# Kernel optimization log

Hardware: AMD Instinct MI355X
Metric: run time of the kernel (lower is better)

Reference implementation:

```python
import jax, jax.numpy as jnp
import numpy as np

B = 8192        # number of drug-cell pairs (graphs)
NPG = 32        # nodes per graph
EPG = 64        # directed edges per graph
N = B * NPG     # total nodes
E = B * EPG     # total edges
CELL = 908      # cell_inp_dim
BN_EPS = 1e-5


def _bn(x):
    # BatchNorm1d in training mode with gamma=1, beta=0 (fresh init), biased var
    m = x.mean(0)
    v = x.var(0)
    return (x - m) * jax.lax.rsqrt(v + BN_EPS)


def _lin_params(k, fan_in, fan_out):
    kw, _ = jax.random.split(k)
    w = jax.random.normal(kw, (fan_in, fan_out), jnp.float32) / np.sqrt(fan_in)
    b = jnp.zeros((fan_out,), jnp.float32)
    return w, b


_DIMS = [("ce_1", CELL, 516), ("ce_2", 516, 256), ("ce_3", 256, 128),
         ("g1_1", 9, 128), ("g1_2", 128, 128),
         ("g2_1", 128, 128), ("g2_2", 128, 128),
         ("d_1", 128, 128), ("d_2", 128, 128),
         ("f_1", 256, 128), ("f_2", 128, 64), ("f_3", 64, 1)]


def setup_inputs() -> dict:
    key = jax.random.key(0)
    ks = jax.random.split(key, 4 + len(_DIMS))
    inp = {}
    inp["cell"] = jax.random.normal(ks[0], (B, CELL), jnp.float32)
    inp["drug_x"] = jax.random.normal(ks[1], (N, 9), jnp.float32)
    g = jnp.arange(E) // EPG  # graph id per edge
    src = g * NPG + jax.random.randint(ks[2], (E,), 0, NPG)
    dst = g * NPG + jax.random.randint(ks[3], (E,), 0, NPG)
    inp["drug_edge_index"] = jnp.stack([src, dst]).astype(jnp.int32)
    inp["drug_batch"] = (jnp.arange(N) // NPG).astype(jnp.int32)
    for i, (nm, a, b) in enumerate(_DIMS):
        w, bb = _lin_params(ks[4 + i], a, b)
        inp[nm + "_w"] = w
        inp[nm + "_b"] = bb
    return inp


def _forward(cell, drug_x, src, dst, batch,
             ce_1_w, ce_1_b, ce_2_w, ce_2_b, ce_3_w, ce_3_b,
             g1_1_w, g1_1_b, g1_2_w, g1_2_b,
             g2_1_w, g2_1_b, g2_2_w, g2_2_b,
             d_1_w, d_1_b, d_2_w, d_2_b,
             f_1_w, f_1_b, f_2_w, f_2_b, f_3_w, f_3_b):
    # cell_emb branch (dropout = identity in eval/reference)
    c = jax.nn.relu(_bn(cell @ ce_1_w + ce_1_b))
    c = jax.nn.relu(_bn(c @ ce_2_w + ce_2_b))
    c = jax.nn.relu(_bn(c @ ce_3_w + ce_3_b))

    # GINConv 1: h = MLP((1+eps)*x + sum_{j in N(i)} x_j), eps=0
    agg = jax.ops.segment_sum(drug_x[src], dst, num_segments=N)
    h = drug_x + agg
    h = jax.nn.relu(_bn(h @ g1_1_w + g1_1_b)) @ g1_2_w + g1_2_b  # inner MLP: Lin-BN-ReLU-Lin
    h = _bn(jax.nn.relu(h))  # outer ReLU then BN (per Sequential order)

    # GINConv 2
    agg = jax.ops.segment_sum(h[src], dst, num_segments=N)
    h = h + agg
    h = jax.nn.relu(_bn(h @ g2_1_w + g2_1_b)) @ g2_2_w + g2_2_b
    h = _bn(jax.nn.relu(h))

    # global max pool over nodes of each graph -> [B, 128]
    p = jax.ops.segment_max(h, batch, num_segments=B)

    d = jax.nn.relu(_bn(p @ d_1_w + d_1_b))
    d = jax.nn.relu(d @ d_2_w + d_2_b)

    z = jnp.concatenate([c, d], axis=-1)  # [B, 256]
    z = jax.nn.elu(_bn(z @ f_1_w + f_1_b))
    z = jax.nn.elu(_bn(z @ f_2_w + f_2_b))
    y = (z @ f_3_w + f_3_b).reshape(B)
    return y


def reference(cell, drug_x, drug_edge_index, drug_batch,
              ce_1_w, ce_1_b, ce_2_w, ce_2_b, ce_3_w, ce_3_b,
              g1_1_w, g1_1_b, g1_2_w, g1_2_b,
              g2_1_w, g2_1_b, g2_2_w, g2_2_b,
              d_1_w, d_1_b, d_2_w, d_2_b,
              f_1_w, f_1_b, f_2_w, f_2_b, f_3_w, f_3_b):
    src, dst = drug_edge_index[0], drug_edge_index[1]
    return _forward(cell, drug_x, src, dst, drug_batch,
                    ce_1_w, ce_1_b, ce_2_w, ce_2_b, ce_3_w, ce_3_b,
                    g1_1_w, g1_1_b, g1_2_w, g1_2_b,
                    g2_1_w, g2_1_b, g2_2_w, g2_2_b,
                    d_1_w, d_1_b, d_2_w, d_2_b,
                    f_1_w, f_1_b, f_2_w, f_2_b, f_3_w, f_3_b)
```

## Files before the change

### kernel.cpp

```cpp
#include <hip/hip_runtime.h>
#include <hip/hip_bf16.h>
#include <math.h>

#define BGRAPH 8192
#define NPG 32
#define EPG 64
#define NNODE (BGRAPH * NPG)
#define NEDGE (BGRAPH * EPG)
#define CELLD 908
#define BN_EPS 1e-5f
#define ABF_STR 960
#define C1_STR 576

typedef __attribute__((ext_vector_type(8))) short bf16x8;
typedef __attribute__((ext_vector_type(4))) float f32x4;
typedef __attribute__((ext_vector_type(4))) unsigned short us4;
typedef __attribute__((ext_vector_type(8))) unsigned short us8;

__device__ __forceinline__ unsigned short f2bf(float f)
{
    unsigned int u = __float_as_uint(f);
    u = (u + 0x7FFFu + ((u >> 16) & 1u)) >> 16;
    return (unsigned short)u;
}

__device__ __forceinline__ bf16x8 quant8(const float v[8])
{
    union { bf16x8 b; unsigned short u[8]; } fr;
    #pragma unroll
    for (int j = 0; j < 8; ++j) fr.u[j] = f2bf(v[j]);
    return fr.b;
}

__device__ __forceinline__ void bf2f8(bf16x8 b, float v[8])
{
    union { bf16x8 bb; unsigned short u[8]; } x; x.bb = b;
    #pragma unroll
    for (int j = 0; j < 8; ++j) v[j] = __uint_as_float((unsigned)x.u[j] << 16);
}

__device__ __forceinline__ float apply_in(float v, int mode, float mn, float iv)
{
    if (mode == 1)      { v = (v - mn) * iv; v = fmaxf(v, 0.f); }
    else if (mode == 2) { v = (v - mn) * iv; v = (v > 0.f) ? v : expm1f(v); }
    else if (mode == 3) { v = fmaxf(v, 0.f); v = (v - mn) * iv; }
    return v;
}

struct TransArgs {
    const float* w[11];
    unsigned short* wt[11];
    int K[11], N[11], ntN[11];
    int off[12];
};

__global__ void transpose_w(TransArgs a)
{
    __shared__ float t[64][65];
    int b = blockIdx.x, tid = threadIdx.x;
    int s = 0;
    while (s < 10 && b >= a.off[s + 1]) ++s;
    int t0 = b - a.off[s];
    int K = a.K[s], N = a.N[s], ntn = a.ntN[s];
    int kt = t0 / ntn, nt = t0 - kt * ntn;
    int k0 = kt * 64, n0 = nt * 64;
    const float* w = a.w[s];
    unsigned short* wt = a.wt[s];
    int c = tid & 63, rg = tid >> 6;
    #pragma unroll
    for (int i = 0; i < 16; ++i) {
        int rr = rg * 16 + i;
        int k = k0 + rr, n = n0 + c;
        t[c][rr] = (k < K && n < N) ? w[(size_t)k * N + n] : 0.f;
    }
    __syncthreads();
    #pragma unroll
    for (int i = 0; i < 16; ++i) {
        int rr = rg * 16 + i;
        int n = n0 + rr, k = k0 + c;
        if (n < N && k < K) wt[(size_t)n * K + k] = f2bf(t[rr][c]);
    }
}

struct SetupArgs {
    float* zb; int zTotal; int zBlocks;
    const int* src; const int* dst; int* row_start; int* col_idx;
};

__global__ void setup_all(SetupArgs a)
{
    int b = blockIdx.x;
    int tid = threadIdx.x;
    if (b < a.zBlocks) {
        int i = b * 256 + tid;
        if (i < a.zTotal) a.zb[i] = 0.f;
        return;
    }
    b -= a.zBlocks;
    __shared__ int cnt[4][32], fill[4][32], rsl[4][33];
    int gl = tid >> 6, e = tid & 63;
    int g = b * 4 + gl;
    if (e < 32) { cnt[gl][e] = 0; fill[gl][e] = 0; }
    __syncthreads();
    int s = a.src[g * EPG + e] - g * NPG;
    int d = a.dst[g * EPG + e] - g * NPG;
    atomicAdd(&cnt[gl][d], 1);
    __syncthreads();
    if (e == 0) {
        int acc = 0;
        for (int i = 0; i < 32; ++i) { rsl[gl][i] = acc; acc += cnt[gl][i]; }
        rsl[gl][32] = acc;
    }
    __syncthreads();
    int pos = rsl[gl][d] + atomicAdd(&fill[gl][d], 1);
    a.col_idx[g * EPG + pos] = s;
    if (e < 33) a.row_start[g * 33 + e] = rsl[gl][e];
}

__global__ void quant_cell(const float* __restrict__ cell, unsigned short* __restrict__ abf)
{
    int i = blockIdx.x * 256 + threadIdx.x;
    int row = i / (ABF_STR / 4), c4 = i - row * (ABF_STR / 4);
    int k = c4 * 4;
    us4 w = (us4){0, 0, 0, 0};
    if (k < CELLD) {
        float4 f = *(const float4*)&cell[(size_t)row * CELLD + k];
        w = (us4){ f2bf(f.x), f2bf(f.y), f2bf(f.z), f2bf(f.w) };
    }
    *(us4*)&abf[(size_t)row * ABF_STR + k] = w;
}

__global__ void quant_c1(const float* __restrict__ c1, const float* __restrict__ stats,
                         float inv_sM, unsigned short* __restrict__ out)
{
    int i = blockIdx.x * 256 + threadIdx.x;
    int row = i / (C1_STR / 4), c4 = i - row * (C1_STR / 4);
    int k = c4 * 4;
    us4 w = (us4){0, 0, 0, 0};
    if (k < 516) {
        float4 f = *(const float4*)&c1[(size_t)row * 516 + k];
        float v[4] = {f.x, f.y, f.z, f.w};
        #pragma unroll
        for (int j = 0; j < 4; ++j) {
            float s = stats[k + j], ss = stats[516 + k + j];
            float mn = s * inv_sM;
            float iv = rsqrtf(ss * inv_sM - mn * mn + BN_EPS);
            v[j] = fmaxf((v[j] - mn) * iv, 0.f);
        }
        w = (us4){ f2bf(v[0]), f2bf(v[1]), f2bf(v[2]), f2bf(v[3]) };
    }
    *(us4*)&out[(size_t)row * C1_STR + k] = w;
}

__global__ void reduce_stats(const float* __restrict__ part, int nrows, int nt,
                             float* __restrict__ out)
{
    int c = threadIdx.x;
    int per = nrows >> 6;
    int r0 = blockIdx.x * per;
    bool isq = (c >= 128);
    int cc = isq ? c - 128 : c;
    if (cc >= nt) return;
    float s = 0.f;
    for (int r = 0; r < per; ++r) s += part[(size_t)(r0 + r) * 256 + c];
    unsafeAtomicAdd(&out[(isq ? nt : 0) + cc], s);
}

#define HBS 136

__launch_bounds__(256)
__global__ void gin_s1(const float* __restrict__ drug_x,
                       const int* __restrict__ row_start,
                       const int* __restrict__ col_idx,
                       const unsigned short* __restrict__ W11,
                       const float* __restrict__ b11,
                       unsigned short* uout,
                       float* __restrict__ part)
{
    __shared__ __align__(16) unsigned short h[4 * 32 * HBS];
    __shared__ __align__(16) unsigned char ubuf[4096];
    __shared__ int rs[4][36];
    __shared__ int ci[4][64];

    unsigned short* w11l = (unsigned short*)ubuf;
    float* red = (float*)ubuf;

    int tid  = threadIdx.x;
    int wave = tid >> 6;
    int lane = tid & 63;
    int quad = lane >> 4;
    int l16  = lane & 15;
    int g0   = blockIdx.x * 4;
    unsigned short* hw = h + wave * (32 * HBS);
    float* xw = (float*)hw;

    for (int i = tid; i < 128 * 16; i += 256) {
        int n = i >> 4, k = i & 15;
        w11l[i] = (k < 9) ? W11[n * 9 + k] : (unsigned short)0;
    }
    if (tid < 132) {
        int gl = tid / 33, idx = tid - gl * 33;
        rs[gl][idx] = row_start[(g0 + gl) * 33 + idx];
    }
    {
        int gl = tid >> 6, e = tid & 63;
        ci[gl][e] = col_idx[(g0 + gl) * EPG + e];
    }
    {
        const float* xg = drug_x + (size_t)(g0 + wave) * 32 * 9;
        for (int i = lane; i < 32 * 16; i += 64) {
            int rr = i >> 4, c = i & 15;
            xw[i] = (c < 9) ? xg[rr * 9 + c] : 0.f;
        }
    }
    __syncthreads();

    f32x4 acc[2][8];
    #pragma unroll
    for (int i = 0; i < 2; ++i)
        #pragma unroll
        for (int j = 0; j < 8; ++j)
            acc[i][j] = (f32x4){0.f, 0.f, 0.f, 0.f};

    {
        bf16x8 af[2];
        #pragma unroll
        for (int mt = 0; mt < 2; ++mt) {
            int rowl = mt * 16 + l16;
            float v[8] = {0, 0, 0, 0, 0, 0, 0, 0};
            if (quad < 2) {
                float4 lo = *(const float4*)&xw[rowl * 16 + quad * 8];
                float4 hi = *(const float4*)&xw[rowl * 16 + quad * 8 + 4];
                v[0] = lo.x; v[1] = lo.y; v[2] = lo.z; v[3] = lo.w;
                v[4] = hi.x; v[5] = hi.y; v[6] = hi.z; v[7] = hi.w;
                int e0 = rs[wave][rowl], e1 = rs[wave][rowl + 1];
                for (int e = e0; e < e1; ++e) {
                    int sr = ci[wave][e];
                    float4 l2 = *(const float4*)&xw[sr * 16 + quad * 8];
                    float4 h2 = *(const float4*)&xw[sr * 16 + quad * 8 + 4];
                    v[0] += l2.x; v[1] += l2.y; v[2] += l2.z; v[3] += l2.w;
                    v[4] += h2.x; v[5] += h2.y; v[6] += h2.z; v[7] += h2.w;
                }
            }
            af[mt] = quant8(v);
        }
        #pragma unroll
        for (int nt = 0; nt < 8; ++nt) {
            bf16x8 b;
            if (quad < 2) b = *(const bf16x8*)(const void*)&w11l[(nt * 16 + l16) * 16 + quad * 8];
            else { float z[8] = {0,0,0,0,0,0,0,0}; b = quant8(z); }
            acc[0][nt] = __builtin_amdgcn_mfma_f32_16x16x32_bf16(af[0], b, acc[0][nt], 0, 0, 0);
            acc[1][nt] = __builtin_amdgcn_mfma_f32_16x16x32_bf16(af[1], b, acc[1][nt], 0, 0, 0);
        }
    }

    float ls[8], lq[8];
    unsigned short* ub = uout + (size_t)(g0 + wave) * 32 * 128;
    #pragma unroll
    for (int nt = 0; nt < 8; ++nt) {
        int col = nt * 16 + l16;
        float bv = b11[col];
        float s0 = 0.f, q0 = 0.f;
        #pragma unroll
        for (int mt = 0; mt < 2; ++mt) {
            int rb = mt * 16 + quad * 4;
            #pragma unroll
            for (int r = 0; r < 4; ++r) {
                float u = acc[mt][nt][r] + bv;
                ub[(size_t)(rb + r) * 128 + col] = f2bf(u);
                s0 += u; q0 += u * u;
            }
        }
        ls[nt] = s0; lq[nt] = q0;
    }
    __syncthreads();
    #pragma unroll
    for (int nt = 0; nt < 8; ++nt) {
        float s = ls[nt], q = lq[nt];
        s += __shfl_xor(s, 16); q += __shfl_xor(q, 16);
        s += __shfl_xor(s, 32); q += __shfl_xor(q, 32);
        if (quad == 0) {
            int col = nt * 16 + l16;
            red[(wave * 2 + 0) * 128 + col] = s;
            red[(wave * 2 + 1) * 128 + col] = q;
        }
    }
    __syncthreads();
    if (tid < 128) {
        float s = red[0 * 128 + tid] + red[2 * 128 + tid] + red[4 * 128 + tid] + red[6 * 128 + tid];
        float q = red[1 * 128 + tid] + red[3 * 128 + tid] + red[5 * 128 + tid] + red[7 * 128 + tid];
        part[(size_t)blockIdx.x * 256 + tid] = s;
        part[(size_t)blockIdx.x * 256 + 128 + tid] = q;
    }
}

__launch_bounds__(256)
__global__ void gin_s3f(const unsigned short* __restrict__ uin,
                        const int* __restrict__ row_start,
                        const int* __restrict__ col_idx,
                        const unsigned short* __restrict__ Wt,
                        const float* __restrict__ bias,
                        const float* __restrict__ in_stats, float inv_sM,
                        unsigned short* __restrict__ uout,
                        float* __restrict__ part)
{
    __shared__ __align__(16) unsigned short wsl[128 * 136];
    __shared__ float pmv[256];
    __shared__ int rs[2][33];
    __shared__ int ci[2][64];
    float* zt = (float*)wsl;

    int tid  = threadIdx.x;
    int wave = tid >> 6;
    int lane = tid & 63;
    int quad = lane >> 4;
    int l16  = lane & 15;
    int g0   = blockIdx.x * 2;
    int row0 = blockIdx.x * 64;

    if (tid < 128) {
        float s = in_stats[tid], ss = in_stats[128 + tid];
        float mn = s * inv_sM;
        pmv[tid] = mn;
        pmv[128 + tid] = rsqrtf(ss * inv_sM - mn * mn + BN_EPS);
    }
    if (tid < 66) {
        int gl = tid / 33, idx = tid - gl * 33;
        rs[gl][idx] = row_start[(g0 + gl) * 33 + idx];
    }
    if (tid >= 128) {
        int t = tid - 128;
        ci[t >> 6][t & 63] = col_idx[(g0 + (t >> 6)) * EPG + (t & 63)];
    }
    for (int i = tid; i < 128 * 32; i += 256) {
        int n = i >> 5, k = (i & 31) * 4;
        *(us4*)&wsl[n * 136 + k] = *(const us4*)&Wt[(size_t)n * 128 + k];
    }
    __syncthreads();

    bf16x8 afrag[4];
    {
        const unsigned short* ap = uin + (size_t)(row0 + wave * 16 + l16) * 128;
        #pragma unroll
        for (int ks = 0; ks < 4; ++ks) {
            int kb = ks * 32 + quad * 8;
            float v[8];
            bf2f8(*(const bf16x8*)(const void*)&ap[kb], v);
            #pragma unroll
            for (int j = 0; j < 8; ++j)
                v[j] = (fmaxf(v[j], 0.f) - pmv[kb + j]) * pmv[128 + kb + j];
            afrag[ks] = quant8(v);
        }
    }

    f32x4 acc[8];
    #pragma unroll
    for (int j = 0; j < 8; ++j) acc[j] = (f32x4){0.f, 0.f, 0.f, 0.f};
    #pragma unroll
    for (int ks = 0; ks < 4; ++ks) {
        int kb = ks * 32 + quad * 8;
        #pragma unroll
        for (int nt = 0; nt < 8; ++nt) {
            bf16x8 b = *(const bf16x8*)(const void*)&wsl[(nt * 16 + l16) * 136 + kb];
            acc[nt] = __builtin_amdgcn_mfma_f32_16x16x32_bf16(afrag[ks], b, acc[nt], 0, 0, 0);
        }
    }
    __syncthreads();

    #pragma unroll
    for (int nt = 0; nt < 8; ++nt) {
        int col = nt * 16 + l16;
        #pragma unroll
        for (int r = 0; r < 4; ++r)
            zt[(wave * 16 + quad * 4 + r) * 132 + col] = acc[nt][r];
    }
    __syncthreads();

    float sv[4] = {0.f, 0.f, 0.f, 0.f}, qv[4] = {0.f, 0.f, 0.f, 0.f};
    {
        int c4  = (tid & 31) * 4;
        int rg  = tid >> 5;
        int hh  = rg >> 2;
        int rb0 = (rg & 3) * 8;
        float4 bv = *(const float4*)&bias[c4];
        unsigned short* ub = uout + (size_t)row0 * 128;
        for (int rr = 0; rr < 8; ++rr) {
            int r = rb0 + rr;
            int lr = hh * 32 + r;
            float4 val = *(const float4*)&zt[lr * 132 + c4];
            int e0 = rs[hh][r], e1 = rs[hh][r + 1];
            for (int e = e0; e < e1; ++e) {
                float4 zz = *(const float4*)&zt[(hh * 32 + ci[hh][e]) * 132 + c4];
                val.x += zz.x; val.y += zz.y; val.z += zz.z; val.w += zz.w;
            }
            float u0 = val.x + bv.x, u1 = val.y + bv.y;
            float u2 = val.z + bv.z, u3 = val.w + bv.w;
            *(us4*)&ub[(size_t)lr * 128 + c4] =
                (us4){ f2bf(u0), f2bf(u1), f2bf(u2), f2bf(u3) };
            sv[0] += u0; sv[1] += u1; sv[2] += u2; sv[3] += u3;
            qv[0] += u0 * u0; qv[1] += u1 * u1; qv[2] += u2 * u2; qv[3] += u3 * u3;
        }
    }
    __syncthreads();
    {
        int c4 = (tid & 31) * 4, rg = tid >> 5;
        #pragma unroll
        for (int j = 0; j < 4; ++j) {
            zt[rg * 128 + c4 + j] = sv[j];
            zt[1024 + rg * 128 + c4 + j] = qv[j];
        }
    }
    __syncthreads();
    if (tid < 128) {
        float s = 0.f, q = 0.f;
        #pragma unroll
        for (int rg = 0; rg < 8; ++rg) {
            s += zt[rg * 128 + tid];
            q += zt[1024 + rg * 128 + tid];
        }
        part[(size_t)blockIdx.x * 256 + tid] = s;
        part[(size_t)blockIdx.x * 256 + 128 + tid] = q;
    }
}

template<int DO_POOL>
__launch_bounds__(256)
__global__ void gin_lin(const unsigned short* __restrict__ uin,
                        const unsigned short* __restrict__ Wt,
                        const float* __restrict__ bias,
                        const float* __restrict__ in_stats, float inv_sM,
                        unsigned short* uout,
                        float* __restrict__ part,
                        float* __restrict__ pool_out)
{
    __shared__ __align__(16) unsigned short Ws_l[128 * 136];
    __shared__ float pmv[256];
    __shared__ float red[4][2][128];

    int tid  = threadIdx.x;
    int wave = tid >> 6;
    int lane = tid & 63;
    int quad = lane >> 4;
    int l16  = lane & 15;
    int row0 = blockIdx.x * 64;

    for (int i = tid; i < 128 * 32; i += 256) {
        int n = i >> 5, k = (i & 31) * 4;
        *(us4*)&Ws_l[n * 136 + k] = *(const us4*)&Wt[(size_t)n * 128 + k];
    }
    if (tid < 128) {
        float s = in_stats[tid], ss = in_stats[128 + tid];
        float mn = s * inv_sM;
        pmv[tid] = mn;
        pmv[128 + tid] = rsqrtf(ss * inv_sM - mn * mn + BN_EPS);
    }
    __syncthreads();

    bf16x8 afrag[4];
    {
        const unsigned short* ap = uin + (size_t)(row0 + wave * 16 + l16) * 128;
        #pragma unroll
        for (int ks = 0; ks < 4; ++ks) {
            int kb = ks * 32 + quad * 8;
            float v[8];
            bf2f8(*(const bf16x8*)(const void*)&ap[kb], v);
            #pragma unroll
            for (int j = 0; j < 8; ++j)
                v[j] = fmaxf((v[j] - pmv[kb + j]) * pmv[128 + kb + j], 0.f);
            afrag[ks] = quant8(v);
        }
    }

    f32x4 acc[8];
    #pragma unroll
    for (int j = 0; j < 8; ++j) acc[j] = (f32x4){0.f, 0.f, 0.f, 0.f};
    #pragma unroll
    for (int ks = 0; ks < 4; ++ks) {
        int kb = ks * 32 + quad * 8;
        #pragma unroll
        for (int nt = 0; nt < 8; ++nt) {
            bf16x8 b = *(const bf16x8*)(const void*)&Ws_l[(nt * 16 + l16) * 136 + kb];
            acc[nt] = __builtin_amdgcn_mfma_f32_16x16x32_bf16(afrag[ks], b, acc[nt], 0, 0, 0);
        }
    }

    float ls[8], lq[8], lm[8];
    #pragma unroll
    for (int nt = 0; nt < 8; ++nt) {
        int col = nt * 16 + l16;
        float bv = bias[col];
        int rb = row0 + wave * 16 + quad * 4;
        float s0 = 0.f, q0 = 0.f, mx = -INFINITY;
        #pragma unroll
        for (int r = 0; r < 4; ++r) {
            float u = acc[nt][r] + bv;
            float ru = fmaxf(u, 0.f);
            s0 += ru; q0 += ru * ru;
            if (DO_POOL) mx = fmaxf(mx, ru);
            else uout[(size_t)(rb + r) * 128 + col] = f2bf(u);
        }
        ls[nt] = s0; lq[nt] = q0; lm[nt] = mx;
    }

    #pragma unroll
    for (int nt = 0; nt < 8; ++nt) {
        float s = ls[nt], q = lq[nt];
        s += __shfl_xor(s, 16); q += __shfl_xor(q, 16);
        s += __shfl_xor(s, 32); q += __shfl_xor(q, 32);
        if (quad == 0) {
            red[wave][0][nt * 16 + l16] = s;
            red[wave][1][nt * 16 + l16] = q;
        }
    }
    __syncthreads();
    if (tid < 128) {
        float s = red[0][0][tid] + red[1][0][tid] + red[2][0][tid] + red[3][0][tid];
        float q = red[0][1][tid] + red[1][1][tid] + red[2][1][tid] + red[3][1][tid];
        part[(size_t)blockIdx.x * 256 + tid] = s;
        part[(size_t)blockIdx.x * 256 + 128 + tid] = q;
    }
    if (DO_POOL) {
        __syncthreads();
        #pragma unroll
        for (int nt = 0; nt < 8; ++nt) {
            float m = lm[nt];
            m = fmaxf(m, __shfl_xor(m, 16));
            m = fmaxf(m, __shfl_xor(m, 32));
            if (quad == 0) red[wave][0][nt * 16 + l16] = m;
        }
        __syncthreads();
        {
            int gi = tid >> 7, col = tid & 127;
            float m = fmaxf(red[gi * 2][0][col], red[gi * 2 + 1][0][col]);
            pool_out[(size_t)((row0 >> 5) + gi) * 128 + col] = m;
        }
    }
}

template<int KSTEPS, int NT>
__launch_bounds__(256)
__global__ void gemm_rB(const float* __restrict__ A, const float* __restrict__ A2,
                        int lda, int K, int stats_K, int ksplit,
                        const unsigned short* __restrict__ Wt,
                        const float* __restrict__ bias, float* __restrict__ C,
                        const float* __restrict__ in_stats, float inv_sM, int in_mode,
                        float* __restrict__ part, int stats_mode, int out_act)
{
    constexpr int LSTRW = KSTEPS * 32 + 8;
    constexpr int NSUBW = NT / 64;
    __shared__ unsigned short Ws_l[NT * LSTRW];
    __shared__ float pm[KSTEPS * 32], pv[KSTEPS * 32];

    int tid  = threadIdx.x;
    int wave = tid >> 6;
    int lane = tid & 63;
    int quad = lane >> 4;
    int l16  = lane & 15;
    int m0   = blockIdx.x * 16;

    for (int i = tid; i < NT * (KSTEPS * 8); i += 256) {
        int n = i / (KSTEPS * 8), g4 = i % (KSTEPS * 8);
        int k = g4 * 4;
        us4 w = (us4){0, 0, 0, 0};
        if (k < K) w = *(const us4*)(Wt + (size_t)n * K + k);
        *(us4*)&Ws_l[n * LSTRW + k] = w;
    }
    if (in_mode) {
        for (int k = tid; k < KSTEPS * 32; k += 256) {
            float mn = 0.f, iv = 1.f;
            if (k < stats_K) {
                float s = in_stats[k], ss = in_stats[stats_K + k];
                mn = s * inv_sM;
                float vr = ss * inv_sM - mn * mn;
                iv = rsqrtf(vr + BN_EPS);
            }
            pm[k] = mn; pv[k] = iv;
        }
    }
    __syncthreads();

    bf16x8 afrag[KSTEPS];
    {
        int row = m0 + l16;
        const float* ap = A + (size_t)row * lda;
        #pragma unroll
        for (int ks = 0; ks < KSTEPS; ++ks) {
            int kb = ks * 32 + quad * 8;
            float v[8];
            #pragma unroll
            for (int hh = 0; hh < 2; ++hh) {
                int k = kb + hh * 4;
                const float* p = (k >= ksplit) ? &A2[(size_t)row * 128 + (k - 128)]
                                               : &ap[k];
                float4 f = *(const float4*)p;
                v[hh * 4 + 0] = f.x; v[hh * 4 + 1] = f.y;
                v[hh * 4 + 2] = f.z; v[hh * 4 + 3] = f.w;
            }
            if (in_mode) {
                #pragma unroll
                for (int j = 0; j < 8; ++j)
                    v[j] = apply_in(v[j], in_mode, pm[kb + j], pv[kb + j]);
            }
            afrag[ks] = quant8(v);
        }
    }

    f32x4 acc[NSUBW];
    #pragma unroll
    for (int j = 0; j < NSUBW; ++j) acc[j] = (f32x4){0.f, 0.f, 0.f, 0.f};

    #pragma unroll
    for (int ks = 0; ks < KSTEPS; ++ks) {
        #pragma unroll
        for (int nt = 0; nt < NSUBW; ++nt) {
            bf16x8 b = *(const bf16x8*)(const void*)
                &Ws_l[((wave * NSUBW + nt) * 16 + l16) * LSTRW + ks * 32 + quad * 8];
            acc[nt] = __builtin_amdgcn_mfma_f32_16x16x32_bf16(afrag[ks], b, acc[nt], 0, 0, 0);
        }
    }

    float ls[NSUBW], lq[NSUBW];
    #pragma unroll
    for (int nt = 0; nt < NSUBW; ++nt) { ls[nt] = 0.f; lq[nt] = 0.f; }

    #pragma unroll
    for (int nt = 0; nt < NSUBW; ++nt) {
        int col = (wave * NSUBW + nt) * 16 + l16;
        float bv = bias[col];
        int rbase = m0 + quad * 4;
        #pragma unroll
        for (int r = 0; r < 4; ++r) {
            float u = acc[nt][r] + bv;
            if (C) {
                float wv = out_act ? fmaxf(u, 0.f) : u;
                C[(size_t)(rbase + r) * NT + col] = wv;
            }
            if (stats_mode) {
                float s = (stats_mode == 2) ? fmaxf(u, 0.f) : u;
                ls[nt] += s; lq[nt] += s * s;
            }
        }
    }

    if (stats_mode) {
        #pragma unroll
        for (int nt = 0; nt < NSUBW; ++nt) {
            float s = ls[nt], q = lq[nt];
            s += __shfl_xor(s, 16); q += __shfl_xor(q, 16);
            s += __shfl_xor(s, 32); q += __shfl_xor(q, 32);
            if (quad == 0) {
                int col = (wave * NSUBW + nt) * 16 + l16;
                part[(size_t)blockIdx.x * 256 + col] = s;
                part[(size_t)blockIdx.x * 256 + 128 + col] = q;
            }
        }
    }
}

template<int NT, int ABF>
__launch_bounds__(256)
__global__ void gemm_cell(const float* __restrict__ A,
                          const unsigned short* __restrict__ Abf, int abf_str,
                          const unsigned short* __restrict__ Wt,
                          const float* __restrict__ bias, float* __restrict__ C,
                          int M, int K, int N,
                          const float* __restrict__ in_stats, float inv_sM, int in_mode,
                          float* __restrict__ out_stats)
{
    constexpr int NSUB = NT / 16;
    constexpr int PMSZ = ABF ? 1 : 916;
    __shared__ unsigned short As_l[64 * 72];
    __shared__ unsigned short Ws_l[NT * 72];
    __shared__ float pm[PMSZ], pv[PMSZ];
    __shared__ float red[4][2][NT];

    int tid = threadIdx.x;
    int wave = tid >> 6;
    int lane = tid & 63;
    int quad = lane >> 4;
    int l16 = lane & 15;
    int m0 = blockIdx.x * 64, n0 = blockIdx.y * NT;

    if (!ABF && in_mode) {
        for (int k = tid; k < K; k += 256) {
            float s = in_stats[k], ss = in_stats[K + k];
            float mn = s * inv_sM;
            float vr = ss * inv_sM - mn * mn;
            pm[k] = mn; pv[k] = rsqrtf(vr + BN_EPS);
        }
        __syncthreads();
    }

    f32x4 acc[NSUB];
    #pragma unroll
    for (int j = 0; j < NSUB; ++j) acc[j] = (f32x4){0.f, 0.f, 0.f, 0.f};

    for (int k0 = 0; k0 < K; k0 += 64) {
        if (ABF) {
            #pragma unroll
            for (int t = 0; t < 2; ++t) {
                int i = t * 256 + tid;
                int row = i >> 3, c8 = (i & 7) * 8;
                us8 w = *(const us8*)&Abf[(size_t)(m0 + row) * abf_str + k0 + c8];
                *(us8*)&As_l[row * 72 + c8] = w;
            }
        } else {
            for (int i = tid; i < 64 * 16; i += 256) {
                int row = i >> 4, f4 = i & 15;
                int k = k0 + f4 * 4;
                us4 w4 = (us4){0, 0, 0, 0};
                if (k < K) {
                    float4 f = *(const float4*)&A[(size_t)(m0 + row) * K + k];
                    if (in_mode) {
                        f.x = apply_in(f.x, in_mode, pm[k], pv[k]);
                        f.y = apply_in(f.y, in_mode, pm[k + 1], pv[k + 1]);
                        f.z = apply_in(f.z, in_mode, pm[k + 2], pv[k + 2]);
                        f.w = apply_in(f.w, in_mode, pm[k + 3], pv[k + 3]);
                    }
                    w4 = (us4){ f2bf(f.x), f2bf(f.y), f2bf(f.z), f2bf(f.w) };
                }
                *(us4*)&As_l[row * 72 + f4 * 4] = w4;
            }
        }
        for (int i = tid; i < NT * 16; i += 256) {
            int nn = i >> 4, kt = i & 15;
            int k = k0 + kt * 4;
            int gn = n0 + nn;
            us4 w4 = (us4){0, 0, 0, 0};
            if (gn < N && k < K) w4 = *(const us4*)&Wt[(size_t)gn * K + k];
            *(us4*)&Ws_l[nn * 72 + kt * 4] = w4;
        }
        __syncthreads();
        int rowb = wave * 16;
        #pragma unroll
        for (int ks = 0; ks < 2; ++ks) {
            bf16x8 a = *(const bf16x8*)(const void*)&As_l[(rowb + l16) * 72 + ks * 32 + quad * 8];
            #pragma unroll
            for (int nt = 0; nt < NSUB; ++nt) {
                bf16x8 b = *(const bf16x8*)(const void*)&Ws_l[(nt * 16 + l16) * 72 + ks * 32 + quad * 8];
                acc[nt] = __builtin_amdgcn_mfma_f32_16x16x32_bf16(a, b, acc[nt], 0, 0, 0);
            }
        }
        __syncthreads();
    }

    float ls[NSUB], lq[NSUB];
    #pragma unroll
    for (int nt = 0; nt < NSUB; ++nt) { ls[nt] = 0.f; lq[nt] = 0.f; }

    #pragma unroll
    for (int nt = 0; nt < NSUB; ++nt) {
        int col = n0 + nt * 16 + l16;
        if (col < N) {
            float bv = bias[col];
            int rbase = m0 + wave * 16 + quad * 4;
            #pragma unroll
            for (int r = 0; r < 4; ++r) {
                float u = acc[nt][r] + bv;
                C[(size_t)(rbase + r) * N + col] = u;
                ls[nt] += u; lq[nt] += u * u;
            }
        }
    }

    #pragma unroll
    for (int nt = 0; nt < NSUB; ++nt) {
        float s = ls[nt], q = lq[nt];
        s += __shfl_xor(s, 16); q += __shfl_xor(q, 16);
        s += __shfl_xor(s, 32); q += __shfl_xor(q, 32);
        if (quad == 0) { red[wave][0][nt * 16 + l16] = s; red[wave][1][nt * 16 + l16] = q; }
    }
    __syncthreads();
    if (tid < NT) {
        int col = n0 + tid;
        if (col < N) {
            float s = red[0][0][tid] + red[1][0][tid] + red[2][0][tid] + red[3][0][tid];
            float q = red[0][1][tid] + red[1][1][tid] + red[2][1][tid] + red[3][1][tid];
            unsafeAtomicAdd(&out_stats[col], s);
            unsafeAtomicAdd(&out_stats[N + col], q);
        }
    }
}

__global__ void final_dot(const float* __restrict__ u, const float* __restrict__ w,
                          const float* __restrict__ b, float* __restrict__ y,
                          const float* __restrict__ stats, float inv_sM)
{
    __shared__ float pmv[64], piv[64], sw[64];
    int tid = threadIdx.x;
    if (tid < 64) {
        float s = stats[tid], ss = stats[64 + tid];
        float mn = s * inv_sM;
        float vr = ss * inv_sM - mn * mn;
        pmv[tid] = mn;
        piv[tid] = rsqrtf(vr + BN_EPS);
        sw[tid] = w[tid];
    }
    __syncthreads();
    int i = blockIdx.x * blockDim.x + tid;
    if (i >= BGRAPH) return;
    float acc = 0.f;
    #pragma unroll
    for (int k = 0; k < 64; ++k) {
        float v = (u[(size_t)i * 64 + k] - pmv[k]) * piv[k];
        v = (v > 0.f) ? v : expm1f(v);
        acc += v * sw[k];
    }
    y[i] = acc + b[0];
}

extern "C" void kernel_launch(void* const* d_in, const int* in_sizes, int n_in,
                              void* d_out, int out_size, void* d_ws, size_t ws_size,
                              hipStream_t stream)
{
    const float* cell   = (const float*)d_in[0];
    const float* drug_x = (const float*)d_in[1];
    const int*   eidx   = (const int*)d_in[2];
    const float* ce1w = (const float*)d_in[4];  const float* ce1b = (const float*)d_in[5];
    const float* ce2w = (const float*)d_in[6];  const float* ce2b = (const float*)d_in[7];
    const float* ce3w = (const float*)d_in[8];  const float* ce3b = (const float*)d_in[9];
    const float* g11w = (const float*)d_in[10]; const float* g11b = (const float*)d_in[11];
    const float* g12w = (const float*)d_in[12]; const float* g12b = (const float*)d_in[13];
    const float* g21w = (const float*)d_in[14]; const float* g21b = (const float*)d_in[15];
    const float* g22w = (const float*)d_in[16]; const float* g22b = (const float*)d_in[17];
    const float* d1w  = (const float*)d_in[18]; const float* d1b  = (const float*)d_in[19];
    const float* d2w  = (const float*)d_in[20]; const float* d2b  = (const float*)d_in[21];
    const float* f1w  = (const float*)d_in[22]; const float* f1b  = (const float*)d_in[23];
    const float* f2w  = (const float*)d_in[24]; const float* f2b  = (const float*)d_in[25];
    const float* f3w  = (const float*)d_in[26]; const float* f3b  = (const float*)d_in[27];

    const int* src = eidx;
    const int* dst = eidx + NEDGE;
    float* out = (float*)d_out;

    const float INV_N = 1.f / (float)NNODE;
    const float INV_B = 1.f / (float)BGRAPH;
    const int KBIG = 1 << 30;

    float* ws = (float*)d_ws;
    unsigned short* ubg = (unsigned short*)ws;
    float* pbuf = ws + (size_t)NNODE * 64;
    float* sb   = pbuf + (size_t)BGRAPH * 128;
    unsigned short* wtb = (unsigned short*)(sb + 10 * 1032);
    auto ST = [&](int i) { return sb + (size_t)i * 1032; };
    float* st_u1    = ST(0);
    float* st_u2rel = ST(1);
    float* st_u3    = ST(2);
    float* st_u4rel = ST(3);
    float* st_c1    = ST(4);
    float* st_c2    = ST(5);
    float* st_c3    = ST(6);
    float* st_d1    = ST(7);
    float* st_f1    = ST(8);
    float* st_f2    = ST(9);

    float* c1    = ws;
    float* c2    = c1 + (size_t)BGRAPH * 516;
    float* c3u   = c2 + (size_t)BGRAPH * 256;
    float* dbuf  = c3u + (size_t)BGRAPH * 128;
    float* d2buf = dbuf + (size_t)BGRAPH * 128;
    float* f1o   = d2buf + (size_t)BGRAPH * 128;
    float* f2o   = f1o + (size_t)BGRAPH * 128;

    struct WDef { const float* w; int K; int N; };
    WDef wd[11] = {
        {ce1w, CELLD, 516}, {ce2w, 516, 256}, {ce3w, 256, 128},
        {g11w, 9, 128}, {g12w, 128, 128}, {g21w, 128, 128}, {g22w, 128, 128},
        {d1w, 128, 128}, {d2w, 128, 128}, {f1w, 256, 128}, {f2w, 128, 64}
    };
    TransArgs ta;
    int off = 0;
    unsigned short* wt[11];
    ta.off[0] = 0;
    for (int i = 0; i < 11; ++i) {
        wt[i] = wtb + off;
        ta.w[i] = wd[i].w; ta.wt[i] = wt[i];
        ta.K[i] = wd[i].K; ta.N[i] = wd[i].N;
        ta.ntN[i] = (wd[i].N + 63) / 64;
        ta.off[i + 1] = ta.off[i] + ((wd[i].K + 63) / 64) * ta.ntN[i];
        off += wd[i].K * wd[i].N;
    }

    SetupArgs sa;
    sa.zb = sb; sa.zTotal = 10 * 1032; sa.zBlocks = (10 * 1032 + 255) / 256;
    sa.src = src; sa.dst = dst;

    int csr_off = (off + 7) & ~7;
    int* row_start = (int*)(wtb + csr_off);
    int* col_idx   = row_start + (size_t)BGRAPH * 33;
    float* part = (float*)(col_idx + (size_t)NEDGE);
    unsigned short* Abf  = (unsigned short*)(part + (size_t)4096 * 256);
    unsigned short* C1bf = Abf + (size_t)BGRAPH * ABF_STR;
    sa.row_start = row_start; sa.col_idx = col_idx;

    transpose_w<<<ta.off[11], 256, 0, stream>>>(ta);
    setup_all<<<sa.zBlocks + BGRAPH / 4, 256, 0, stream>>>(sa);

    gin_s1<<<BGRAPH / 4, 256, 0, stream>>>(
        drug_x, row_start, col_idx, wt[3], g11b, ubg, part);
    reduce_stats<<<64, 256, 0, stream>>>(part, BGRAPH / 4, 128, st_u1);

    gin_lin<0><<<NNODE / 64, 256, 0, stream>>>(
        ubg, wt[4], g12b, st_u1, INV_N, ubg, part, nullptr);
    reduce_stats<<<64, 256, 0, stream>>>(part, NNODE / 64, 128, st_u2rel);

    gin_s3f<<<BGRAPH / 2, 256, 0, stream>>>(
        ubg, row_start, col_idx, wt[5], g21b, st_u2rel, INV_N, ubg, part);
    reduce_stats<<<64, 256, 0, stream>>>(part, BGRAPH / 2, 128, st_u3);

    gin_lin<1><<<NNODE / 64, 256, 0, stream>>>(
        ubg, wt[6], g22b, st_u3, INV_N, nullptr, part, pbuf);
    reduce_stats<<<64, 256, 0, stream>>>(part, NNODE / 64, 128, st_u4rel);

    quant_cell<<<(BGRAPH * (ABF_STR / 4)) / 256, 256, 0, stream>>>(cell, Abf);
    gemm_cell<128, 1><<<dim3(BGRAPH / 64, 5), 256, 0, stream>>>(
        nullptr, Abf, ABF_STR, wt[0], ce1b, c1, BGRAPH, CELLD, 516,
        nullptr, 0.f, 0, st_c1);
    quant_c1<<<(BGRAPH * (C1_STR / 4)) / 256, 256, 0, stream>>>(c1, st_c1, INV_B, C1bf);
    gemm_cell<64, 1><<<dim3(BGRAPH / 64, 4), 256, 0, stream>>>(
        nullptr, C1bf, C1_STR, wt[1], ce2b, c2, BGRAPH, 516, 256,
        nullptr, 0.f, 0, st_c2);
    gemm_rB<8, 128><<<BGRAPH / 16, 256, 0, stream>>>(
        c2, nullptr, 256, 256, 256, KBIG, wt[2], ce3b, c3u,
        st_c2, INV_B, 1, part, 1, 0);
    reduce_stats<<<64, 256, 0, stream>>>(part, BGRAPH / 16, 128, st_c3);

    gemm_rB<4, 128><<<BGRAPH / 16, 256, 0, stream>>>(
        pbuf, nullptr, 128, 128, 128, KBIG, wt[7], d1b, dbuf,
        st_u4rel, INV_N, 3, part, 1, 0);
    reduce_stats<<<64, 256, 0, stream>>>(part, BGRAPH / 16, 128, st_d1);
    gemm_rB<4, 128><<<BGRAPH / 16, 256, 0, stream>>>(
        dbuf, nullptr, 128, 128, 128, KBIG, wt[8], d2b, d2buf,
        st_d1, INV_B, 1, part, 0, 1);

    gemm_rB<8, 128><<<BGRAPH / 16, 256, 0, stream>>>(
        c3u, d2buf, 128, 256, 128, 128, wt[9], f1b, f1o,
        st_c3, INV_B, 1, part, 1, 0);
    reduce_stats<<<64, 256, 0, stream>>>(part, BGRAPH / 16, 128, st_f1);
    gemm_rB<4, 64><<<BGRAPH / 16, 256, 0, stream>>>(
        f1o, nullptr, 128, 128, 128, KBIG, wt[10], f2b, f2o,
        st_f1, INV_B, 2, part, 1, 0);
    reduce_stats<<<64, 256, 0, stream>>>(part, BGRAPH / 16, 64, st_f2);
    final_dot<<<BGRAPH / 256, 256, 0, stream>>>(f2o, f3w, f3b, out, st_f2, INV_B);
}
```

Measured before the change: 567.1 us.

## Read gemm_rB weights directly from global and shrink gemm_cell M-tile to 32

gemm_rB no longer stages the weight matrix into shared memory. Each wave loads its B fragments straight from global memory, which is expected to hit in L2, and the barrier is now taken only when input-normalization stats are computed. gemm_cell moves from 64-row to 32-row tiles with a 2x2 wave split over M and N, which doubles the grid size and halves the shared-memory footprint. The aim is to cut per-block staging and LDS overhead and to raise occupancy and parallelism, at the cost of uncoalesced global weight reads and less A/W reuse per block.

```diff
diff --git a/kernel.cpp b/kernel.cpp
--- a/kernel.cpp
+++ b/kernel.cpp
@@ -546,9 +546,7 @@
                         const float* __restrict__ in_stats, float inv_sM, int in_mode,
                         float* __restrict__ part, int stats_mode, int out_act)
 {
-    constexpr int LSTRW = KSTEPS * 32 + 8;
     constexpr int NSUBW = NT / 64;
-    __shared__ unsigned short Ws_l[NT * LSTRW];
     __shared__ float pm[KSTEPS * 32], pv[KSTEPS * 32];
 
     int tid  = threadIdx.x;
@@ -558,13 +556,6 @@
     int l16  = lane & 15;
     int m0   = blockIdx.x * 16;
 
-    for (int i = tid; i < NT * (KSTEPS * 8); i += 256) {
-        int n = i / (KSTEPS * 8), g4 = i % (KSTEPS * 8);
-        int k = g4 * 4;
-        us4 w = (us4){0, 0, 0, 0};
-        if (k < K) w = *(const us4*)(Wt + (size_t)n * K + k);
-        *(us4*)&Ws_l[n * LSTRW + k] = w;
-    }
     if (in_mode) {
         for (int k = tid; k < KSTEPS * 32; k += 256) {
             float mn = 0.f, iv = 1.f;
@@ -576,8 +567,8 @@
             }
             pm[k] = mn; pv[k] = iv;
         }
-    }
-    __syncthreads();
+        __syncthreads();
+    }
 
     bf16x8 afrag[KSTEPS];
     {
@@ -613,8 +604,8 @@
     for (int ks = 0; ks < KSTEPS; ++ks) {
         #pragma unroll
         for (int nt = 0; nt < NSUBW; ++nt) {
-            bf16x8 b = *(const bf16x8*)(const void*)
-                &Ws_l[((wave * NSUBW + nt) * 16 + l16) * LSTRW + ks * 32 + quad * 8];
+            int wrow = (wave * NSUBW + nt) * 16 + l16;
+            bf16x8 b = *(const bf16x8*)(const void*)&Wt[(size_t)wrow * K + ks * 32 + quad * 8];
             acc[nt] = __builtin_amdgcn_mfma_f32_16x16x32_bf16(afrag[ks], b, acc[nt], 0, 0, 0);
         }
     }
@@ -667,19 +658,20 @@
                           const float* __restrict__ in_stats, float inv_sM, int in_mode,
                           float* __restrict__ out_stats)
 {
-    constexpr int NSUB = NT / 16;
+    constexpr int NSUB = NT / 32;
     constexpr int PMSZ = ABF ? 1 : 916;
-    __shared__ unsigned short As_l[64 * 72];
+    __shared__ unsigned short As_l[32 * 72];
     __shared__ unsigned short Ws_l[NT * 72];
     __shared__ float pm[PMSZ], pv[PMSZ];
-    __shared__ float red[4][2][NT];
+    __shared__ float red[2][2][NT];
 
     int tid = threadIdx.x;
     int wave = tid >> 6;
     int lane = tid & 63;
     int quad = lane >> 4;
     int l16 = lane & 15;
-    int m0 = blockIdx.x * 64, n0 = blockIdx.y * NT;
+    int mhalf = wave & 1, nhalf = wave >> 1;
+    int m0 = blockIdx.x * 32, n0 = blockIdx.y * NT;
 
     if (!ABF && in_mode) {
         for (int k = tid; k < K; k += 256) {
@@ -697,15 +689,11 @@
 
     for (int k0 = 0; k0 < K; k0 += 64) {
         if (ABF) {
-            #pragma unroll
-            for (int t = 0; t < 2; ++t) {
-                int i = t * 256 + tid;
-                int row = i >> 3, c8 = (i & 7) * 8;
-                us8 w = *(const us8*)&Abf[(size_t)(m0 + row) * abf_str + k0 + c8];
-                *(us8*)&As_l[row * 72 + c8] = w;
-            }
+            int row = tid >> 3, c8 = (tid & 7) * 8;
+            us8 w = *(const us8*)&Abf[(size_t)(m0 + row) * abf_str + k0 + c8];
+            *(us8*)&As_l[row * 72 + c8] = w;
         } else {
-            for (int i = tid; i < 64 * 16; i += 256) {
+            for (int i = tid; i < 32 * 16; i += 256) {
                 int row = i >> 4, f4 = i & 15;
                 int k = k0 + f4 * 4;
                 us4 w4 = (us4){0, 0, 0, 0};
@@ -731,13 +719,13 @@
             *(us4*)&Ws_l[nn * 72 + kt * 4] = w4;
         }
         __syncthreads();
-        int rowb = wave * 16;
         #pragma unroll
         for (int ks = 0; ks < 2; ++ks) {
-            bf16x8 a = *(const bf16x8*)(const void*)&As_l[(rowb + l16) * 72 + ks * 32 + quad * 8];
+            bf16x8 a = *(const bf16x8*)(const void*)&As_l[(mhalf * 16 + l16) * 72 + ks * 32 + quad * 8];
             #pragma unroll
             for (int nt = 0; nt < NSUB; ++nt) {
-                bf16x8 b = *(const bf16x8*)(const void*)&Ws_l[(nt * 16 + l16) * 72 + ks * 32 + quad * 8];
+                bf16x8 b = *(const bf16x8*)(const void*)
+                    &Ws_l[(nhalf * (NT / 2) + nt * 16 + l16) * 72 + ks * 32 + quad * 8];
                 acc[nt] = __builtin_amdgcn_mfma_f32_16x16x32_bf16(a, b, acc[nt], 0, 0, 0);
             }
         }
@@ -750,10 +738,10 @@
 
     #pragma unroll
     for (int nt = 0; nt < NSUB; ++nt) {
-        int col = n0 + nt * 16 + l16;
+        int col = n0 + nhalf * (NT / 2) + nt * 16 + l16;
         if (col < N) {
             float bv = bias[col];
-            int rbase = m0 + wave * 16 + quad * 4;
+            int rbase = m0 + mhalf * 16 + quad * 4;
             #pragma unroll
             for (int r = 0; r < 4; ++r) {
                 float u = acc[nt][r] + bv;
@@ -768,14 +756,18 @@
         float s = ls[nt], q = lq[nt];
         s += __shfl_xor(s, 16); q += __shfl_xor(q, 16);
         s += __shfl_xor(s, 32); q += __shfl_xor(q, 32);
-        if (quad == 0) { red[wave][0][nt * 16 + l16] = s; red[wave][1][nt * 16 + l16] = q; }
+        if (quad == 0) {
+            int lc = nhalf * (NT / 2) + nt * 16 + l16;
+            red[mhalf][0][lc] = s;
+            red[mhalf][1][lc] = q;
+        }
     }
     __syncthreads();
     if (tid < NT) {
         int col = n0 + tid;
         if (col < N) {
-            float s = red[0][0][tid] + red[1][0][tid] + red[2][0][tid] + red[3][0][tid];
-            float q = red[0][1][tid] + red[1][1][tid] + red[2][1][tid] + red[3][1][tid];
+            float s = red[0][0][tid] + red[1][0][tid];
+            float q = red[0][1][tid] + red[1][1][tid];
             unsafeAtomicAdd(&out_stats[col], s);
             unsafeAtomicAdd(&out_stats[N + col], q);
         }
@@ -913,11 +905,11 @@
     reduce_stats<<<64, 256, 0, stream>>>(part, NNODE / 64, 128, st_u4rel);
 
     quant_cell<<<(BGRAPH * (ABF_STR / 4)) / 256, 256, 0, stream>>>(cell, Abf);
-    gemm_cell<128, 1><<<dim3(BGRAPH / 64, 5), 256, 0, stream>>>(
+    gemm_cell<128, 1><<<dim3(BGRAPH / 32, 5), 256, 0, stream>>>(
         nullptr, Abf, ABF_STR, wt[0], ce1b, c1, BGRAPH, CELLD, 516,
         nullptr, 0.f, 0, st_c1);
     quant_c1<<<(BGRAPH * (C1_STR / 4)) / 256, 256, 0, stream>>>(c1, st_c1, INV_B, C1bf);
-    gemm_cell<64, 1><<<dim3(BGRAPH / 64, 4), 256, 0, stream>>>(
+    gemm_cell<64, 1><<<dim3(BGRAPH / 32, 4), 256, 0, stream>>>(
         nullptr, C1bf, C1_STR, wt[1], ce2b, c2, BGRAPH, 516, 256,
         nullptr, 0.f, 0, st_c2);
     gemm_rB<8, 128><<<BGRAPH / 16, 256, 0, stream>>>(
```

After: 553.2 us. 2.5% less time.
